# Optimization experiments

Measured on AMD Instinct MI355X. Metric: run time of the kernel, lower is better.

Reference implementation:

```python
import jax, jax.numpy as jnp
import numpy as np

NDIM = (256, 256, 256)
NMIN = (-1.0, -1.0, -1.0)
NMAX = (1.0, 1.0, 1.0)
NDELTA = tuple((NMAX[i] - NMIN[i]) / (NDIM[i] - 1.0) for i in range(3))
MIN_DEG, MAX_DEG = 0, 10
ANNEALED_ALPHA = 1.0
EPS = 1e-12


def compute_grad(grid):
    # central differences on the voxel grid with edge padding -> [N, 3]
    g = grid.reshape(NDIM[0], NDIM[1], NDIM[2])
    p = jnp.pad(g, ((1, 1), (1, 1), (1, 1)), mode='edge')
    dx = (p[2:, 1:-1, 1:-1] - p[:-2, 1:-1, 1:-1]) / (2.0 * NDELTA[0])
    dy = (p[1:-1, 2:, 1:-1] - p[1:-1, :-2, 1:-1]) / (2.0 * NDELTA[1])
    dz = (p[1:-1, 1:-1, 2:] - p[1:-1, 1:-1, :-2]) / (2.0 * NDELTA[2])
    return jnp.stack([dx, dy, dz], axis=-1).reshape(-1, 3)


def trilinear3(data, pts):
    # data: [N, 4] flattened voxel features, pts: [B, 3] -> [B, 4]
    x = (pts[..., 0] - NMIN[0]) / NDELTA[0]
    y = (pts[..., 1] - NMIN[1]) / NDELTA[1]
    z = (pts[..., 2] - NMIN[2]) / NDELTA[2]
    x0f = jnp.floor(x); y0f = jnp.floor(y); z0f = jnp.floor(z)
    xd = (x - x0f)[..., None]
    yd = (y - y0f)[..., None]
    zd = (z - z0f)[..., None]
    x0 = jnp.clip(x0f.astype(jnp.int32), 0, NDIM[0] - 1)
    x1 = jnp.clip(x0f.astype(jnp.int32) + 1, 0, NDIM[0] - 1)
    y0 = jnp.clip(y0f.astype(jnp.int32), 0, NDIM[1] - 1)
    y1 = jnp.clip(y0f.astype(jnp.int32) + 1, 0, NDIM[1] - 1)
    z0 = jnp.clip(z0f.astype(jnp.int32), 0, NDIM[2] - 1)
    z1 = jnp.clip(z0f.astype(jnp.int32) + 1, 0, NDIM[2] - 1)
    sYZ, sZ = NDIM[1] * NDIM[2], NDIM[2]
    gat = lambda i, j, k: data[sYZ * i + sZ * j + k]
    c00 = gat(x0, y0, z0) * (1 - xd) + gat(x1, y0, z0) * xd
    c01 = gat(x0, y0, z1) * (1 - xd) + gat(x1, y0, z1) * xd
    c10 = gat(x0, y1, z0) * (1 - xd) + gat(x1, y1, z0) * xd
    c11 = gat(x0, y1, z1) * (1 - xd) + gat(x1, y1, z1) * xd
    c0 = c00 * (1 - yd) + c10 * yd
    c1 = c01 * (1 - yd) + c11 * yd
    return c0 * (1 - zd) + c1 * zd


def annealed_pos_enc(x, alpha):
    # nerfies-style windowed positional encoding with identity concat
    bands = jnp.arange(MIN_DEG, MAX_DEG, dtype=x.dtype)  # [D]
    scales = 2.0 ** bands
    xb = x[..., None, :] * scales[:, None]               # [..., D, 3]
    four = jnp.sin(jnp.stack([xb, xb + 0.5 * jnp.pi], axis=-2))  # [..., D, 2, 3]
    w = jnp.clip(alpha - bands, 0.0, 1.0)
    w = 0.5 * (1.0 - jnp.cos(jnp.pi * w))                # cosine easing window
    four = four * w[:, None, None]
    four = four.reshape(x.shape[:-1] + (-1,))            # [..., D*6]
    return jnp.concatenate([x, four], axis=-1)           # [..., 3 + D*6]


def mlp(feats, w0, b0, w1, b1, w2, b2, w3, b3, wo, bo):
    # net_depth=4, skip_layer=2 -> concat inputs after layer index 2
    h = jax.nn.relu(feats @ w0 + b0)
    h = jax.nn.relu(h @ w1 + b1)
    h = jax.nn.relu(h @ w2 + b2)
    h = jnp.concatenate([h, feats], axis=-1)
    h = jax.nn.relu(h @ w3 + b3)
    return h @ wo + bo


def safe_l2_norm(v):
    return jnp.sqrt(jnp.sum(v * v, axis=-1, keepdims=True) + EPS)


def setup_inputs() -> dict:
    key = jax.random.key(0)
    ks = jax.random.split(key, 8)
    B = 1048576
    N = NDIM[0] * NDIM[1] * NDIM[2]
    x = jax.random.uniform(ks[0], (B, 3), jnp.float32, -1.0, 1.0)
    grid = jax.random.normal(ks[1], (N, 1), jnp.float32)
    glorot = lambda k, fi, fo: jax.random.normal(k, (fi, fo), jnp.float32) * jnp.sqrt(2.0 / (fi + fo))
    return {
        'x': x, 'grid': grid,
        'w0': glorot(ks[2], 63, 128), 'b0': jnp.zeros((128,), jnp.float32),
        'w1': glorot(ks[3], 128, 128), 'b1': jnp.zeros((128,), jnp.float32),
        'w2': glorot(ks[4], 128, 128), 'b2': jnp.zeros((128,), jnp.float32),
        'w3': glorot(ks[5], 191, 128), 'b3': jnp.zeros((128,), jnp.float32),
        'wo': jax.random.normal(ks[6], (128, 3), jnp.float32) * 1e-5,  # output_init normal(1e-5)
        'bo': jnp.zeros((3,), jnp.float32),
    }


def reference(x, grid, w0, b0, w1, b1, w2, b2, w3, b3, wo, bo):
    data = jnp.concatenate([grid, compute_grad(grid)], axis=-1)  # [N, 4]
    ret = trilinear3(data, x)                                    # [B, 4]
    feats = annealed_pos_enc(x[:, None], ANNEALED_ALPHA * MAX_DEG)  # [B, 1, 63]
    raw = mlp(feats, w0, b0, w1, b1, w2, b2, w3, b3, wo, bo)[:, 0]  # [B, 3]
    # residual + direct output: rotate gradient vector by axis-angle raw
    theta = safe_l2_norm(raw)
    e = raw / theta
    cond = ret[..., 1:]
    a = safe_l2_norm(cond)
    v = cond / a
    rot = a * (jnp.cos(theta) * v + jnp.sin(theta) * jnp.cross(e, v)
               + (1.0 - jnp.cos(theta)) * jnp.sum(e * v, axis=-1, keepdims=True) * e)
    return (ret[..., :1], ret[..., 1:], rot)
```

## Files before the change

### kernel.cpp

```cpp
#include <hip/hip_runtime.h>


typedef __attribute__((ext_vector_type(4))) float f4;
typedef long long llg;
typedef __attribute__((ext_vector_type(2))) long long llg2;

#define MFMA8 __builtin_amdgcn_mfma_f32_16x16x32_fp8_fp8
#define SCHED_FENCE() __builtin_amdgcn_sched_barrier(0)

__device__ __forceinline__ float bf2f(unsigned int u) {
    union { float f; unsigned int i; } v; v.i = u << 16; return v.f;
}
__device__ __forceinline__ unsigned int pkbf(float a, float b) {
    unsigned int r;
    asm("v_cvt_pk_bf16_f32 %0, %1, %2" : "=v"(r) : "v"(a), "v"(b));
    return r;
}
__device__ __forceinline__ float vfract(float a) {
    float d; asm("v_fract_f32 %0, %1" : "=v"(d) : "v"(a)); return d;
}
__device__ __forceinline__ float vsin(float a) {
    float d; asm("v_sin_f32 %0, %1" : "=v"(d) : "v"(a)); return d;
}
__device__ __forceinline__ float gv(const float* __restrict__ g, int i, int j, int k) {
    return g[(i * 256 + j) * 256 + k];
}
__device__ __forceinline__ int featmap(int kp) {
    if (kp < 3) return kp;
    if (kp == 3) return -1;
    const int m = kp - 4, b = m / 6, r = m - 6 * b, d = r >> 1, c = r & 1;
    return 3 + 6 * b + 3 * c + d;
}
__device__ __forceinline__ int hidperm(int k) {
    const int kt = k >> 5, q = (k >> 3) & 3, j = k & 7;
    return 32 * kt + ((j >> 2) << 4) + (q << 2) + (j & 3);
}
__device__ __forceinline__ llg mkllg(unsigned int lo, unsigned int hi) {
    return (llg)(((unsigned long long)lo) | (((unsigned long long)hi) << 32));
}
__device__ __forceinline__ unsigned int pack8(f4 acc) {
    int d = __builtin_amdgcn_cvt_pk_fp8_f32(fmaxf(acc[0], 0.f), fmaxf(acc[1], 0.f), 0, false);
    d     = __builtin_amdgcn_cvt_pk_fp8_f32(fmaxf(acc[2], 0.f), fmaxf(acc[3], 0.f), d, true);
    return (unsigned int)d;
}

#define WS_TOTAL 67584
#define SWZ_BLOCKS 264
#define DG_BLOCKS 8192
#define DG_OFF_SH 131072
#define WS_NEED (262144ull + 16777216ull * 8ull)
#define WO_SCALE 8192.0f
#define WO_INV   (1.0f / 8192.0f)
#define INV2PI 0.15915494309189535f

__global__ __launch_bounds__(256) void prep(
    const float* __restrict__ g,
    const float* __restrict__ w0, const float* __restrict__ w1,
    const float* __restrict__ w2, const float* __restrict__ w3,
    const float* __restrict__ wo,
    unsigned char* __restrict__ ws8, unsigned short* __restrict__ dg,
    int do_dgrid)
{
    const int bid = blockIdx.x;
    if (bid < SWZ_BLOCKS) {
        int idx = bid * 256 + threadIdx.x;
        const float* src; int base, KTP, Kact, Nact, ld;
        if (idx < 8192)       { src = w0; base = 0;     KTP = 1; Kact = 64;  Nact = 128; ld = 128; }
        else if (idx < 24576) { src = w1; base = 8192;  KTP = 2; Kact = 128; Nact = 128; ld = 128; }
        else if (idx < 40960) { src = w2; base = 24576; KTP = 2; Kact = 128; Nact = 128; ld = 128; }
        else if (idx < 65536) { src = w3; base = 40960; KTP = 3; Kact = 192; Nact = 128; ld = 128; }
        else                  { src = wo; base = 65536; KTP = 2; Kact = 128; Nact = 3;   ld = 3;   }
        int local = idx - base;
        int j    = local & 7;
        int half = (local >> 3) & 1;
        int lane = (local >> 4) & 63;
        int c    = local >> 10;
        int ktp  = c % KTP, nt = c / KTP;
        int kt   = ktp * 2 + half;
        int k = kt * 32 + ((lane >> 4) << 3) + j;
        int n = nt * 16 + (lane & 15);
        float v = 0.0f;
        if (k < Kact && n < Nact) {
            int ko;
            if (base == 0) {
                ko = featmap(k);
            } else if (base == 40960) {
                if (k >= 128) {
                    int f = featmap(k - 128);
                    ko = (f < 0) ? -1 : 128 + f;
                } else {
                    ko = hidperm(k);
                }
            } else {
                ko = hidperm(k);
            }
            if (ko >= 0) v = src[ko * ld + n];
            if (base == 65536) v *= WO_SCALE;
        }
        int p = __builtin_amdgcn_cvt_pk_fp8_f32(v, v, 0, false);
        ws8[idx] = (unsigned char)(p & 0xff);
    } else if (do_dgrid) {
        const int t  = (bid - SWZ_BLOCKS) * 256 + threadIdx.x;
        const int k0 = (t & 31) << 3;
        const int j  = (t >> 5) & 255;
        const int i  = t >> 13;
        const float* row = g + (i * 256 + j) * 256;
        const float* rxp = g + (min(i + 1, 255) * 256 + j) * 256;
        const float* rxm = g + (max(i - 1, 0)   * 256 + j) * 256;
        const float* ryp = g + (i * 256 + min(j + 1, 255)) * 256;
        const float* rym = g + (i * 256 + max(j - 1, 0))   * 256;
        float se[8], sxp[8], sxm[8], syp[8], sym[8];
        {
            f4 a = *(const f4*)(row + k0), b = *(const f4*)(row + k0 + 4);
            #pragma unroll
            for (int q = 0; q < 4; ++q) { se[q] = a[q]; se[q + 4] = b[q]; }
            a = *(const f4*)(rxp + k0); b = *(const f4*)(rxp + k0 + 4);
            #pragma unroll
            for (int q = 0; q < 4; ++q) { sxp[q] = a[q]; sxp[q + 4] = b[q]; }
            a = *(const f4*)(rxm + k0); b = *(const f4*)(rxm + k0 + 4);
            #pragma unroll
            for (int q = 0; q < 4; ++q) { sxm[q] = a[q]; sxm[q + 4] = b[q]; }
            a = *(const f4*)(ryp + k0); b = *(const f4*)(ryp + k0 + 4);
            #pragma unroll
            for (int q = 0; q < 4; ++q) { syp[q] = a[q]; syp[q + 4] = b[q]; }
            a = *(const f4*)(rym + k0); b = *(const f4*)(rym + k0 + 4);
            #pragma unroll
            for (int q = 0; q < 4; ++q) { sym[q] = a[q]; sym[q + 4] = b[q]; }
        }
        float zv[10];
        zv[0] = row[max(k0 - 1, 0)];
        #pragma unroll
        for (int q = 0; q < 8; ++q) zv[q + 1] = se[q];
        zv[9] = row[min(k0 + 8, 255)];
        unsigned int o[16];
        #pragma unroll
        for (int q = 0; q < 8; ++q) {
            o[q * 2 + 0] = pkbf(se[q], (sxp[q] - sxm[q]) * 63.75f);
            o[q * 2 + 1] = pkbf((syp[q] - sym[q]) * 63.75f, (zv[q + 2] - zv[q]) * 63.75f);
        }
        unsigned short* dst = dg + (size_t)(((i * 256 + j) * 256 + k0)) * 4;
        #pragma unroll
        for (int q = 0; q < 4; ++q)
            *(uint4*)(dst + q * 8) = *(const uint4*)(&o[q * 4]);
    }
}

#define FSTRIDE_B 88
#define WV_BYTES (32 * FSTRIDE_B)

#define HIDDEN_LAYER(WSL, BIASP, SRCP, DSTP)                                    \
    do {                                                                        \
        _Pragma("unroll")                                                       \
        for (int utp = 0; utp < 4; ++utp) {                                     \
            const int utA = 2 * utp, utB = 2 * utp + 1;                         \
            llg2 wa0 = *(const llg2*)((WSL) + ((utA * 2 + 0) * 64 + lane) * 16);\
            llg2 wa1 = *(const llg2*)((WSL) + ((utA * 2 + 1) * 64 + lane) * 16);\
            llg2 wb0 = *(const llg2*)((WSL) + ((utB * 2 + 0) * 64 + lane) * 16);\
            llg2 wb1 = *(const llg2*)((WSL) + ((utB * 2 + 1) * 64 + lane) * 16);\
            const f4 biasA = *(const f4*)((BIASP) + utA * 16 + quad * 4);       \
            const f4 biasB = *(const f4*)((BIASP) + utB * 16 + quad * 4);       \
            _Pragma("unroll")                                                   \
            for (int pt = 0; pt < 2; ++pt) {                                    \
                f4 a0 = biasA, a1 = biasB;                                      \
                a0 = MFMA8(wa0[0], SRCP[pt][0], a0, 0, 0, 0);                   \
                a0 = MFMA8(wa0[1], SRCP[pt][1], a0, 0, 0, 0);                   \
                a0 = MFMA8(wa1[0], SRCP[pt][2], a0, 0, 0, 0);                   \
                a0 = MFMA8(wa1[1], SRCP[pt][3], a0, 0, 0, 0);                   \
                a1 = MFMA8(wb0[0], SRCP[pt][0], a1, 0, 0, 0);                   \
                a1 = MFMA8(wb0[1], SRCP[pt][1], a1, 0, 0, 0);                   \
                a1 = MFMA8(wb1[0], SRCP[pt][2], a1, 0, 0, 0);                   \
                a1 = MFMA8(wb1[1], SRCP[pt][3], a1, 0, 0, 0);                   \
                DSTP[pt][utp] = mkllg(pack8(a0), pack8(a1));                    \
            }                                                                   \
            SCHED_FENCE();                                                      \
        }                                                                       \
    } while (0)

template<bool FAST>
__global__ __launch_bounds__(256, 5) void voxmlp(
    const float* __restrict__ x, const float* __restrict__ grid,
    const unsigned char* __restrict__ ws8, const unsigned short* __restrict__ dg,
    const float* __restrict__ b0, const float* __restrict__ b1,
    const float* __restrict__ b2, const float* __restrict__ b3,
    const float* __restrict__ bo,
    float* __restrict__ out, int B)
{
    __shared__ unsigned char smem[WV_BYTES * 4];

    const int lane = threadIdx.x & 63;
    const int wave = threadIdx.x >> 6;
    const int quad = lane >> 4;
    const int lm   = lane & 15;
    unsigned char* fbuf = smem + wave * WV_BYTES;

    const int pbase = blockIdx.x * 128 + wave * 32;

    const int p2   = lane & 31;
    const int role = lane >> 5;
    const int pid  = pbase + p2;

    const float px = x[pid * 3 + 0];
    const float py = x[pid * 3 + 1];
    const float pz = x[pid * 3 + 2];

    if (role == 0) {
        const float fx = (px + 1.0f) * 127.5f;
        const float fy = (py + 1.0f) * 127.5f;
        const float fz = (pz + 1.0f) * 127.5f;
        const float fx0 = floorf(fx), fy0 = floorf(fy), fz0 = floorf(fz);
        const float xd = fx - fx0, yd = fy - fy0, zd = fz - fz0;
        const int ix0 = min(max((int)fx0, 0), 255);
        const int iy0 = min(max((int)fy0, 0), 255);
        const int iz0 = min(max((int)fz0, 0), 255);
        const int ix1 = min(ix0 + 1, 255);
        const int iy1 = min(iy0 + 1, 255);
        const int iz1 = min(iz0 + 1, 255);

        float ret0 = 0.f, c1 = 0.f, c2 = 0.f, c3 = 0.f;
        if (FAST) {
            const unsigned char* dgb = (const unsigned char*)dg;
            const unsigned int vbase = (unsigned int)((ix0 * 65536 + iy0 * 256 + iz0) << 3);
            const unsigned int ox = (unsigned int)((ix1 - ix0) << 19);
            const unsigned int oy = (unsigned int)((iy1 - iy0) << 11);
            const unsigned int oz = (unsigned int)((iz1 - iz0) << 3);
            #pragma unroll
            for (int c = 0; c < 8; ++c) {
                const float wgt = ((c & 4) ? xd : 1.0f - xd) *
                                  ((c & 2) ? yd : 1.0f - yd) *
                                  ((c & 1) ? zd : 1.0f - zd);
                const unsigned int off = vbase + ((c & 4) ? ox : 0u)
                                               + ((c & 2) ? oy : 0u)
                                               + ((c & 1) ? oz : 0u);
                const uint2 w = *(const uint2*)(dgb + off);
                ret0 = fmaf(wgt, bf2f(w.x & 0xffffu), ret0);
                c1   = fmaf(wgt, bf2f(w.x >> 16),     c1);
                c2   = fmaf(wgt, bf2f(w.y & 0xffffu), c2);
                c3   = fmaf(wgt, bf2f(w.y >> 16),     c3);
            }
        } else {
            #pragma unroll
            for (int c = 0; c < 8; ++c) {
                const int i = (c & 4) ? ix1 : ix0;
                const int j = (c & 2) ? iy1 : iy0;
                const int k = (c & 1) ? iz1 : iz0;
                const float wgt = ((c & 4) ? xd : 1.0f - xd) *
                                  ((c & 2) ? yd : 1.0f - yd) *
                                  ((c & 1) ? zd : 1.0f - zd);
                const float v  = gv(grid, i, j, k);
                const float gx = (gv(grid, min(i + 1, 255), j, k) - gv(grid, max(i - 1, 0), j, k)) * 63.75f;
                const float gy = (gv(grid, i, min(j + 1, 255), k) - gv(grid, i, max(j - 1, 0), k)) * 63.75f;
                const float gz = (gv(grid, i, j, min(k + 1, 255)) - gv(grid, i, j, max(k - 1, 0))) * 63.75f;
                ret0 = fmaf(wgt, v,  ret0);
                c1   = fmaf(wgt, gx, c1);
                c2   = fmaf(wgt, gy, c2);
                c3   = fmaf(wgt, gz, c3);
            }
        }
        out[pid] = ret0;
        out[B + pid * 3 + 0] = c1;
        out[B + pid * 3 + 1] = c2;
        out[B + pid * 3 + 2] = c3;
        float* cst = (float*)(fbuf + p2 * FSTRIDE_B + 64);
        cst[0] = c1; cst[1] = c2; cst[2] = c3;
    } else {
        const float r0 = px * INV2PI, r1 = py * INV2PI, r2 = pz * INV2PI;
        unsigned char* fb = fbuf + p2 * FSTRIDE_B;
        auto slotv = [&](int n) -> float {
            if (n == 0) return px;
            if (n == 1) return py;
            if (n == 2) return pz;
            if (n == 3) return 0.0f;
            const int m = n - 4, b = m / 6, t = m % 6, ax = t >> 1, ph = t & 1;
            const float rr = (ax == 0) ? r0 : (ax == 1) ? r1 : r2;
            const float arg = rr * (float)(1 << b) + (ph ? 0.25f : 0.0f);
            return vsin(vfract(arg));
        };
        #pragma unroll
        for (int w = 0; w < 8; ++w) {
            int lo = __builtin_amdgcn_cvt_pk_fp8_f32(slotv(8 * w + 0), slotv(8 * w + 1), 0, false);
            lo     = __builtin_amdgcn_cvt_pk_fp8_f32(slotv(8 * w + 2), slotv(8 * w + 3), lo, true);
            int hi = __builtin_amdgcn_cvt_pk_fp8_f32(slotv(8 * w + 4), slotv(8 * w + 5), 0, false);
            hi     = __builtin_amdgcn_cvt_pk_fp8_f32(slotv(8 * w + 6), slotv(8 * w + 7), hi, true);
            uint2 pk; pk.x = (unsigned int)lo; pk.y = (unsigned int)hi;
            *(uint2*)(fb + w * 8) = pk;
        }
    }
    __builtin_amdgcn_s_barrier();

    const int frow0 = lm * FSTRIDE_B + quad * 8;

    llg actA[2][4];
    llg actB[2][4];
    llg ffp[2][2];

    #pragma unroll
    for (int pt = 0; pt < 2; ++pt)
        #pragma unroll
        for (int kt = 0; kt < 2; ++kt)
            ffp[pt][kt] = *(const llg*)(fbuf + pt * 16 * FSTRIDE_B + frow0 + kt * 32);

    #pragma unroll
    for (int utp = 0; utp < 4; ++utp) {
        const int utA = 2 * utp, utB = 2 * utp + 1;
        llg2 wA = *(const llg2*)(ws8 + (utA * 64 + lane) * 16);
        llg2 wB = *(const llg2*)(ws8 + (utB * 64 + lane) * 16);
        const f4 biasA = *(const f4*)(b0 + utA * 16 + quad * 4);
        const f4 biasB = *(const f4*)(b0 + utB * 16 + quad * 4);
        #pragma unroll
        for (int pt = 0; pt < 2; ++pt) {
            f4 a0 = biasA, a1 = biasB;
            a0 = MFMA8(wA[0], ffp[pt][0], a0, 0, 0, 0);
            a0 = MFMA8(wA[1], ffp[pt][1], a0, 0, 0, 0);
            a1 = MFMA8(wB[0], ffp[pt][0], a1, 0, 0, 0);
            a1 = MFMA8(wB[1], ffp[pt][1], a1, 0, 0, 0);
            actA[pt][utp] = mkllg(pack8(a0), pack8(a1));
        }
        SCHED_FENCE();
    }

    HIDDEN_LAYER(ws8 + 8192,  b1, actA, actB);
    HIDDEN_LAYER(ws8 + 24576, b2, actB, actA);

    #pragma unroll
    for (int utp = 0; utp < 4; ++utp) {
        const int utA = 2 * utp, utB = 2 * utp + 1;
        llg2 ha0 = *(const llg2*)(ws8 + 40960 + ((utA * 3 + 0) * 64 + lane) * 16);
        llg2 ha1 = *(const llg2*)(ws8 + 40960 + ((utA * 3 + 1) * 64 + lane) * 16);
        llg2 ha2 = *(const llg2*)(ws8 + 40960 + ((utA * 3 + 2) * 64 + lane) * 16);
        llg2 hb0 = *(const llg2*)(ws8 + 40960 + ((utB * 3 + 0) * 64 + lane) * 16);
        llg2 hb1 = *(const llg2*)(ws8 + 40960 + ((utB * 3 + 1) * 64 + lane) * 16);
        llg2 hb2 = *(const llg2*)(ws8 + 40960 + ((utB * 3 + 2) * 64 + lane) * 16);
        const f4 biasA = *(const f4*)(b3 + utA * 16 + quad * 4);
        const f4 biasB = *(const f4*)(b3 + utB * 16 + quad * 4);
        #pragma unroll
        for (int pt = 0; pt < 2; ++pt) {
            f4 a0 = biasA, a1 = biasB;
            a0 = MFMA8(ha0[0], actA[pt][0], a0, 0, 0, 0);
            a0 = MFMA8(ha0[1], actA[pt][1], a0, 0, 0, 0);
            a0 = MFMA8(ha1[0], actA[pt][2], a0, 0, 0, 0);
            a0 = MFMA8(ha1[1], actA[pt][3], a0, 0, 0, 0);
            a0 = MFMA8(ha2[0], ffp[pt][0],  a0, 0, 0, 0);
            a0 = MFMA8(ha2[1], ffp[pt][1],  a0, 0, 0, 0);
            a1 = MFMA8(hb0[0], actA[pt][0], a1, 0, 0, 0);
            a1 = MFMA8(hb0[1], actA[pt][1], a1, 0, 0, 0);
            a1 = MFMA8(hb1[0], actA[pt][2], a1, 0, 0, 0);
            a1 = MFMA8(hb1[1], actA[pt][3], a1, 0, 0, 0);
            a1 = MFMA8(hb2[0], ffp[pt][0],  a1, 0, 0, 0);
            a1 = MFMA8(hb2[1], ffp[pt][1],  a1, 0, 0, 0);
            actB[pt][utp] = mkllg(pack8(a0), pack8(a1));
        }
        SCHED_FENCE();
    }

    const llg2 o0 = *(const llg2*)(ws8 + 65536 + (lane * 16));
    const llg2 o1 = *(const llg2*)(ws8 + 65536 + ((64 + lane) * 16));

    const float bo0 = bo[0], bo1 = bo[1], bo2 = bo[2];
    #pragma unroll
    for (int pt = 0; pt < 2; ++pt) {
        f4 acc = {0.f, 0.f, 0.f, 0.f};
        acc = MFMA8(o0[0], actB[pt][0], acc, 0, 0, 0);
        acc = MFMA8(o0[1], actB[pt][1], acc, 0, 0, 0);
        acc = MFMA8(o1[0], actB[pt][2], acc, 0, 0, 0);
        acc = MFMA8(o1[1], actB[pt][3], acc, 0, 0, 0);

        const int pp = pt * 16 + lm;
        const float* cst = (const float*)(fbuf + pp * FSTRIDE_B + 64);
        const float g1 = cst[0], g2 = cst[1], g3 = cst[2];
        const float r0 = acc[0] * WO_INV + bo0;
        const float r1 = acc[1] * WO_INV + bo1;
        const float r2 = acc[2] * WO_INV + bo2;
        const float theta = sqrtf(fmaf(r0, r0, fmaf(r1, r1, r2 * r2)) + 1e-12f);
        const float it = __builtin_amdgcn_rcpf(theta);
        const float e0 = r0 * it, e1 = r1 * it, e2 = r2 * it;
        const float a = sqrtf(fmaf(g1, g1, fmaf(g2, g2, g3 * g3)) + 1e-12f);
        const float ia = __builtin_amdgcn_rcpf(a);
        const float v0 = g1 * ia, v1 = g2 * ia, v2 = g3 * ia;
        const float rv = theta * INV2PI;
        const float st = vsin(vfract(rv));
        const float ct = vsin(vfract(rv + 0.25f));
        const float cx = e1 * v2 - e2 * v1;
        const float cy = e2 * v0 - e0 * v2;
        const float cz = e0 * v1 - e1 * v0;
        const float om = (1.0f - ct) * (e0 * v0 + e1 * v1 + e2 * v2);
        if (quad == 0) {
            const int pid2 = pbase + pp;
            out[4 * B + pid2 * 3 + 0] = a * (ct * v0 + st * cx + om * e0);
            out[4 * B + pid2 * 3 + 1] = a * (ct * v1 + st * cy + om * e1);
            out[4 * B + pid2 * 3 + 2] = a * (ct * v2 + st * cz + om * e2);
        }
    }
}

extern "C" void kernel_launch(void* const* d_in, const int* in_sizes, int n_in,
                              void* d_out, int out_size, void* d_ws, size_t ws_size,
                              hipStream_t stream)
{
    const float* x    = (const float*)d_in[0];
    const float* grid = (const float*)d_in[1];
    const float* w0   = (const float*)d_in[2];
    const float* b0   = (const float*)d_in[3];
    const float* w1   = (const float*)d_in[4];
    const float* b1   = (const float*)d_in[5];
    const float* w2   = (const float*)d_in[6];
    const float* b2   = (const float*)d_in[7];
    const float* w3   = (const float*)d_in[8];
    const float* b3   = (const float*)d_in[9];
    const float* wo   = (const float*)d_in[10];
    const float* bo   = (const float*)d_in[11];
    float* out = (float*)d_out;
    unsigned char* ws8 = (unsigned char*)d_ws;
    unsigned short* dg = (unsigned short*)d_ws + DG_OFF_SH;

    const int B = in_sizes[0] / 3;
    const int fast = (ws_size >= WS_NEED) ? 1 : 0;
    const int nprep = fast ? (SWZ_BLOCKS + DG_BLOCKS) : SWZ_BLOCKS;
    prep<<<nprep, 256, 0, stream>>>(grid, w0, w1, w2, w3, wo, ws8, dg, fast);
    if (fast)
        voxmlp<true><<<B / 128, 256, 0, stream>>>(x, grid, ws8, dg, b0, b1, b2, b3, bo, out, B);
    else
        voxmlp<false><<<B / 128, 256, 0, stream>>>(x, grid, ws8, dg, b0, b1, b2, b3, bo, out, B);
}
```

Measured before the change: 322.1 us.

## Switch MLP matmuls to 16x16x128 scaled FP8 MFMA with new weight layout

Replaces the 16x16x32 FP8 MFMA chains with the gfx950 16x16x128 f8f6f4 scaled MFMA, so each output tile needs one instruction per 128-wide K block instead of four chained ones. The prep kernel re-swizzles the weights into 32-byte-per-lane fragments with a new hidden-unit permutation. The feature row is widened and zero-padded to 128 bytes, with a new ordering for the positional-encoding features. This cuts MFMA issue count and accumulator dependency chains. In exchange, layer 0 and the feature half of layer 3 now multiply zero padding from 64 up to 128, and the feature buffer takes more LDS.

```diff
diff --git a/kernel.cpp b/kernel.cpp
--- a/kernel.cpp
+++ b/kernel.cpp
@@ -4,8 +4,10 @@
 typedef __attribute__((ext_vector_type(4))) float f4;
 typedef long long llg;
 typedef __attribute__((ext_vector_type(2))) long long llg2;
-
-#define MFMA8 __builtin_amdgcn_mfma_f32_16x16x32_fp8_fp8
+typedef __attribute__((ext_vector_type(8))) int v8i;
+
+#define MFMASC(A,B,C) \
+    __builtin_amdgcn_mfma_scale_f32_16x16x128_f8f6f4((A),(B),(C),0,0,0,0x7f,0,0x7f)
 #define SCHED_FENCE() __builtin_amdgcn_sched_barrier(0)
 
 __device__ __forceinline__ float bf2f(unsigned int u) {
@@ -25,27 +27,29 @@
 __device__ __forceinline__ float gv(const float* __restrict__ g, int i, int j, int k) {
     return g[(i * 256 + j) * 256 + k];
 }
-__device__ __forceinline__ int featmap(int kp) {
-    if (kp < 3) return kp;
-    if (kp == 3) return -1;
-    const int m = kp - 4, b = m / 6, r = m - 6 * b, d = r >> 1, c = r & 1;
-    return 3 + 6 * b + 3 * c + d;
-}
-__device__ __forceinline__ int hidperm(int k) {
-    const int kt = k >> 5, q = (k >> 3) & 3, j = k & 7;
-    return 32 * kt + ((j >> 2) << 4) + (q << 2) + (j & 3);
-}
-__device__ __forceinline__ llg mkllg(unsigned int lo, unsigned int hi) {
-    return (llg)(((unsigned long long)lo) | (((unsigned long long)hi) << 32));
+__device__ __forceinline__ int hidperm2(int k) {
+    const int q = k >> 5, m = k & 31, t = m >> 2, j = m & 3;
+    return 16 * t + 4 * q + j;
 }
 __device__ __forceinline__ unsigned int pack8(f4 acc) {
     int d = __builtin_amdgcn_cvt_pk_fp8_f32(fmaxf(acc[0], 0.f), fmaxf(acc[1], 0.f), 0, false);
     d     = __builtin_amdgcn_cvt_pk_fp8_f32(fmaxf(acc[2], 0.f), fmaxf(acc[3], 0.f), d, true);
     return (unsigned int)d;
 }
-
-#define WS_TOTAL 67584
-#define SWZ_BLOCKS 264
+__device__ __forceinline__ v8i ldv8(const unsigned char* p) {
+    union { v8i v; llg2 h[2]; } u;
+    u.h[0] = *(const llg2*)(p);
+    u.h[1] = *(const llg2*)(p + 16);
+    return u.v;
+}
+
+#define L0OFF 0
+#define L1OFF 16384
+#define L2OFF 32768
+#define L3OFF 49152
+#define OUTOFF 81920
+#define WS_TOTAL 83968
+#define SWZ_BLOCKS 328
 #define DG_BLOCKS 8192
 #define DG_OFF_SH 131072
 #define WS_NEED (262144ull + 16777216ull * 8ull)
@@ -64,38 +68,30 @@
     const int bid = blockIdx.x;
     if (bid < SWZ_BLOCKS) {
         int idx = bid * 256 + threadIdx.x;
-        const float* src; int base, KTP, Kact, Nact, ld;
-        if (idx < 8192)       { src = w0; base = 0;     KTP = 1; Kact = 64;  Nact = 128; ld = 128; }
-        else if (idx < 24576) { src = w1; base = 8192;  KTP = 2; Kact = 128; Nact = 128; ld = 128; }
-        else if (idx < 40960) { src = w2; base = 24576; KTP = 2; Kact = 128; Nact = 128; ld = 128; }
-        else if (idx < 65536) { src = w3; base = 40960; KTP = 3; Kact = 192; Nact = 128; ld = 128; }
-        else                  { src = wo; base = 65536; KTP = 2; Kact = 128; Nact = 3;   ld = 3;   }
+        const float* src; int base, KT;
+        if (idx < 16384)      { src = w0; base = L0OFF;  KT = 1; }
+        else if (idx < 32768) { src = w1; base = L1OFF;  KT = 1; }
+        else if (idx < 49152) { src = w2; base = L2OFF;  KT = 1; }
+        else if (idx < 81920) { src = w3; base = L3OFF;  KT = 2; }
+        else                  { src = wo; base = OUTOFF; KT = 1; }
         int local = idx - base;
-        int j    = local & 7;
-        int half = (local >> 3) & 1;
-        int lane = (local >> 4) & 63;
-        int c    = local >> 10;
-        int ktp  = c % KTP, nt = c / KTP;
-        int kt   = ktp * 2 + half;
-        int k = kt * 32 + ((lane >> 4) << 3) + j;
+        int m    = local & 31;
+        int lane = (local >> 5) & 63;
+        int tile = local >> 11;
+        int kb   = (KT == 2) ? (tile & 1) : 0;
+        int nt   = (KT == 2) ? (tile >> 1) : tile;
+        int k = kb * 128 + ((lane >> 4) << 5) + m;
         int n = nt * 16 + (lane & 15);
         float v = 0.0f;
-        if (k < Kact && n < Nact) {
-            int ko;
-            if (base == 0) {
-                ko = featmap(k);
-            } else if (base == 40960) {
-                if (k >= 128) {
-                    int f = featmap(k - 128);
-                    ko = (f < 0) ? -1 : 128 + f;
-                } else {
-                    ko = hidperm(k);
-                }
-            } else {
-                ko = hidperm(k);
-            }
-            if (ko >= 0) v = src[ko * ld + n];
-            if (base == 65536) v *= WO_SCALE;
+        if (base == L0OFF) {
+            if (k < 63) v = src[k * 128 + n];
+        } else if (base == L3OFF) {
+            if (kb == 0) v = src[hidperm2(k) * 128 + n];
+            else { int f = k - 128; if (f < 63) v = src[(128 + f) * 128 + n]; }
+        } else if (base == OUTOFF) {
+            if (n < 3) v = src[hidperm2(k) * 3 + n] * WO_SCALE;
+        } else {
+            v = src[hidperm2(k) * 128 + n];
         }
         int p = __builtin_amdgcn_cvt_pk_fp8_f32(v, v, 0, false);
         ws8[idx] = (unsigned char)(p & 0xff);
@@ -145,36 +141,8 @@
     }
 }
 
-#define FSTRIDE_B 88
+#define FSTRIDE_B 144
 #define WV_BYTES (32 * FSTRIDE_B)
-
-#define HIDDEN_LAYER(WSL, BIASP, SRCP, DSTP)                                    \
-    do {                                                                        \
-        _Pragma("unroll")                                                       \
-        for (int utp = 0; utp < 4; ++utp) {                                     \
-            const int utA = 2 * utp, utB = 2 * utp + 1;                         \
-            llg2 wa0 = *(const llg2*)((WSL) + ((utA * 2 + 0) * 64 + lane) * 16);\
-            llg2 wa1 = *(const llg2*)((WSL) + ((utA * 2 + 1) * 64 + lane) * 16);\
-            llg2 wb0 = *(const llg2*)((WSL) + ((utB * 2 + 0) * 64 + lane) * 16);\
-            llg2 wb1 = *(const llg2*)((WSL) + ((utB * 2 + 1) * 64 + lane) * 16);\
-            const f4 biasA = *(const f4*)((BIASP) + utA * 16 + quad * 4);       \
-            const f4 biasB = *(const f4*)((BIASP) + utB * 16 + quad * 4);       \
-            _Pragma("unroll")                                                   \
-            for (int pt = 0; pt < 2; ++pt) {                                    \
-                f4 a0 = biasA, a1 = biasB;                                      \
-                a0 = MFMA8(wa0[0], SRCP[pt][0], a0, 0, 0, 0);                   \
-                a0 = MFMA8(wa0[1], SRCP[pt][1], a0, 0, 0, 0);                   \
-                a0 = MFMA8(wa1[0], SRCP[pt][2], a0, 0, 0, 0);                   \
-                a0 = MFMA8(wa1[1], SRCP[pt][3], a0, 0, 0, 0);                   \
-                a1 = MFMA8(wb0[0], SRCP[pt][0], a1, 0, 0, 0);                   \
-                a1 = MFMA8(wb0[1], SRCP[pt][1], a1, 0, 0, 0);                   \
-                a1 = MFMA8(wb1[0], SRCP[pt][2], a1, 0, 0, 0);                   \
-                a1 = MFMA8(wb1[1], SRCP[pt][3], a1, 0, 0, 0);                   \
-                DSTP[pt][utp] = mkllg(pack8(a0), pack8(a1));                    \
-            }                                                                   \
-            SCHED_FENCE();                                                      \
-        }                                                                       \
-    } while (0)
 
 template<bool FAST>
 __global__ __launch_bounds__(256, 5) void voxmlp(
@@ -260,7 +228,7 @@
         out[B + pid * 3 + 0] = c1;
         out[B + pid * 3 + 1] = c2;
         out[B + pid * 3 + 2] = c3;
-        float* cst = (float*)(fbuf + p2 * FSTRIDE_B + 64);
+        float* cst = (float*)(fbuf + p2 * FSTRIDE_B + 128);
         cst[0] = c1; cst[1] = c2; cst[2] = c3;
     } else {
         const float r0 = px * INV2PI, r1 = py * INV2PI, r2 = pz * INV2PI;
@@ -269,11 +237,10 @@
             if (n == 0) return px;
             if (n == 1) return py;
             if (n == 2) return pz;
-            if (n == 3) return 0.0f;
-            const int m = n - 4, b = m / 6, t = m % 6, ax = t >> 1, ph = t & 1;
-            const float rr = (ax == 0) ? r0 : (ax == 1) ? r1 : r2;
-            const float arg = rr * (float)(1 << b) + (ph ? 0.25f : 0.0f);
-            return vsin(vfract(arg));
+            if (n >= 63) return 0.0f;
+            const int m = n - 3, b = m / 6, rem = m % 6, s = rem / 3, d = rem % 3;
+            const float rr = (d == 0) ? r0 : (d == 1) ? r1 : r2;
+            return vsin(vfract(rr * (float)(1 << b) + (s ? 0.25f : 0.0f)));
         };
         #pragma unroll
         for (int w = 0; w < 8; ++w) {
@@ -284,88 +251,79 @@
             uint2 pk; pk.x = (unsigned int)lo; pk.y = (unsigned int)hi;
             *(uint2*)(fb + w * 8) = pk;
         }
+        const uint4 z = {0u, 0u, 0u, 0u};
+        #pragma unroll
+        for (int w = 0; w < 4; ++w) *(uint4*)(fb + 64 + w * 16) = z;
     }
     __builtin_amdgcn_s_barrier();
 
-    const int frow0 = lm * FSTRIDE_B + quad * 8;
-
-    llg actA[2][4];
-    llg actB[2][4];
-    llg ffp[2][2];
+    const int frow = lm * FSTRIDE_B + quad * 32;
+
+    v8i actA, actAq;
+    v8i actB, actBq;
+
+    {
+        const v8i f0 = ldv8(fbuf + frow);
+        const v8i f1 = ldv8(fbuf + 16 * FSTRIDE_B + frow);
+        #pragma unroll
+        for (int ut = 0; ut < 8; ++ut) {
+            const v8i w = ldv8(ws8 + L0OFF + (ut * 64 + lane) * 32);
+            const f4 bias = *(const f4*)(b0 + ut * 16 + quad * 4);
+            f4 a0 = MFMASC(w, f0, bias);
+            f4 a1 = MFMASC(w, f1, bias);
+            actA[ut]  = (int)pack8(a0);
+            actAq[ut] = (int)pack8(a1);
+            SCHED_FENCE();
+        }
+    }
 
     #pragma unroll
-    for (int pt = 0; pt < 2; ++pt)
-        #pragma unroll
-        for (int kt = 0; kt < 2; ++kt)
-            ffp[pt][kt] = *(const llg*)(fbuf + pt * 16 * FSTRIDE_B + frow0 + kt * 32);
+    for (int ut = 0; ut < 8; ++ut) {
+        const v8i w = ldv8(ws8 + L1OFF + (ut * 64 + lane) * 32);
+        const f4 bias = *(const f4*)(b1 + ut * 16 + quad * 4);
+        f4 a0 = MFMASC(w, actA,  bias);
+        f4 a1 = MFMASC(w, actAq, bias);
+        actB[ut]  = (int)pack8(a0);
+        actBq[ut] = (int)pack8(a1);
+        SCHED_FENCE();
+    }
 
     #pragma unroll
-    for (int utp = 0; utp < 4; ++utp) {
-        const int utA = 2 * utp, utB = 2 * utp + 1;
-        llg2 wA = *(const llg2*)(ws8 + (utA * 64 + lane) * 16);
-        llg2 wB = *(const llg2*)(ws8 + (utB * 64 + lane) * 16);
-        const f4 biasA = *(const f4*)(b0 + utA * 16 + quad * 4);
-        const f4 biasB = *(const f4*)(b0 + utB * 16 + quad * 4);
-        #pragma unroll
-        for (int pt = 0; pt < 2; ++pt) {
-            f4 a0 = biasA, a1 = biasB;
-            a0 = MFMA8(wA[0], ffp[pt][0], a0, 0, 0, 0);
-            a0 = MFMA8(wA[1], ffp[pt][1], a0, 0, 0, 0);
-            a1 = MFMA8(wB[0], ffp[pt][0], a1, 0, 0, 0);
-            a1 = MFMA8(wB[1], ffp[pt][1], a1, 0, 0, 0);
-            actA[pt][utp] = mkllg(pack8(a0), pack8(a1));
-        }
+    for (int ut = 0; ut < 8; ++ut) {
+        const v8i w = ldv8(ws8 + L2OFF + (ut * 64 + lane) * 32);
+        const f4 bias = *(const f4*)(b2 + ut * 16 + quad * 4);
+        f4 a0 = MFMASC(w, actB,  bias);
+        f4 a1 = MFMASC(w, actBq, bias);
+        actA[ut]  = (int)pack8(a0);
+        actAq[ut] = (int)pack8(a1);
         SCHED_FENCE();
     }
 
-    HIDDEN_LAYER(ws8 + 8192,  b1, actA, actB);
-    HIDDEN_LAYER(ws8 + 24576, b2, actB, actA);
-
-    #pragma unroll
-    for (int utp = 0; utp < 4; ++utp) {
-        const int utA = 2 * utp, utB = 2 * utp + 1;
-        llg2 ha0 = *(const llg2*)(ws8 + 40960 + ((utA * 3 + 0) * 64 + lane) * 16);
-        llg2 ha1 = *(const llg2*)(ws8 + 40960 + ((utA * 3 + 1) * 64 + lane) * 16);
-        llg2 ha2 = *(const llg2*)(ws8 + 40960 + ((utA * 3 + 2) * 64 + lane) * 16);
-        llg2 hb0 = *(const llg2*)(ws8 + 40960 + ((utB * 3 + 0) * 64 + lane) * 16);
-        llg2 hb1 = *(const llg2*)(ws8 + 40960 + ((utB * 3 + 1) * 64 + lane) * 16);
-        llg2 hb2 = *(const llg2*)(ws8 + 40960 + ((utB * 3 + 2) * 64 + lane) * 16);
-        const f4 biasA = *(const f4*)(b3 + utA * 16 + quad * 4);
-        const f4 biasB = *(const f4*)(b3 + utB * 16 + quad * 4);
-        #pragma unroll
-        for (int pt = 0; pt < 2; ++pt) {
-            f4 a0 = biasA, a1 = biasB;
-            a0 = MFMA8(ha0[0], actA[pt][0], a0, 0, 0, 0);
-            a0 = MFMA8(ha0[1], actA[pt][1], a0, 0, 0, 0);
-            a0 = MFMA8(ha1[0], actA[pt][2], a0, 0, 0, 0);
-            a0 = MFMA8(ha1[1], actA[pt][3], a0, 0, 0, 0);
-            a0 = MFMA8(ha2[0], ffp[pt][0],  a0, 0, 0, 0);
-            a0 = MFMA8(ha2[1], ffp[pt][1],  a0, 0, 0, 0);
-            a1 = MFMA8(hb0[0], actA[pt][0], a1, 0, 0, 0);
-            a1 = MFMA8(hb0[1], actA[pt][1], a1, 0, 0, 0);
-            a1 = MFMA8(hb1[0], actA[pt][2], a1, 0, 0, 0);
-            a1 = MFMA8(hb1[1], actA[pt][3], a1, 0, 0, 0);
-            a1 = MFMA8(hb2[0], ffp[pt][0],  a1, 0, 0, 0);
-            a1 = MFMA8(hb2[1], ffp[pt][1],  a1, 0, 0, 0);
-            actB[pt][utp] = mkllg(pack8(a0), pack8(a1));
-        }
-        SCHED_FENCE();
-    }
-
-    const llg2 o0 = *(const llg2*)(ws8 + 65536 + (lane * 16));
-    const llg2 o1 = *(const llg2*)(ws8 + 65536 + ((64 + lane) * 16));
-
+    {
+        const v8i f0 = ldv8(fbuf + frow);
+        const v8i f1 = ldv8(fbuf + 16 * FSTRIDE_B + frow);
+        #pragma unroll
+        for (int ut = 0; ut < 8; ++ut) {
+            const v8i wh = ldv8(ws8 + L3OFF + ((ut * 2 + 0) * 64 + lane) * 32);
+            const v8i wt = ldv8(ws8 + L3OFF + ((ut * 2 + 1) * 64 + lane) * 32);
+            const f4 bias = *(const f4*)(b3 + ut * 16 + quad * 4);
+            f4 a0 = MFMASC(wh, actA,  bias); a0 = MFMASC(wt, f0, a0);
+            f4 a1 = MFMASC(wh, actAq, bias); a1 = MFMASC(wt, f1, a1);
+            actB[ut]  = (int)pack8(a0);
+            actBq[ut] = (int)pack8(a1);
+            SCHED_FENCE();
+        }
+    }
+
+    const v8i wout = ldv8(ws8 + OUTOFF + lane * 32);
     const float bo0 = bo[0], bo1 = bo[1], bo2 = bo[2];
     #pragma unroll
     for (int pt = 0; pt < 2; ++pt) {
         f4 acc = {0.f, 0.f, 0.f, 0.f};
-        acc = MFMA8(o0[0], actB[pt][0], acc, 0, 0, 0);
-        acc = MFMA8(o0[1], actB[pt][1], acc, 0, 0, 0);
-        acc = MFMA8(o1[0], actB[pt][2], acc, 0, 0, 0);
-        acc = MFMA8(o1[1], actB[pt][3], acc, 0, 0, 0);
+        acc = MFMASC(wout, pt ? actBq : actB, acc);
 
         const int pp = pt * 16 + lm;
-        const float* cst = (const float*)(fbuf + pp * FSTRIDE_B + 64);
+        const float* cst = (const float*)(fbuf + pp * FSTRIDE_B + 128);
         const float g1 = cst[0], g2 = cst[1], g3 = cst[2];
         const float r0 = acc[0] * WO_INV + bo0;
         const float r1 = acc[1] * WO_INV + bo1;
```

Result: slower. 349.0 us (+8.3%).

## Balance gather and encoding work across wave halves; halve dgrid prep blocks

Applied to the files above, without the earlier changes.

Before, half of each wave did the 8-corner trilinear gather while the other half computed the sinusoidal feature encoding, so the two halves ran divergent paths. Now both halves do the gather, each taking four corners (one x-slab), and combine partial sums with a cross-lane xor shuffle; then both halves compute half of the encoding slots. The intent is to remove divergence and balance latency between the two lane groups. Separately, the derived-grid prep now runs half as many blocks, each thread processing two voxel rows, which cuts launch and scheduling overhead but lowers parallelism in that phase.

```diff
diff --git a/kernel.cpp b/kernel.cpp
--- a/kernel.cpp
+++ b/kernel.cpp
@@ -46,12 +46,58 @@
 
 #define WS_TOTAL 67584
 #define SWZ_BLOCKS 264
-#define DG_BLOCKS 8192
+#define DG_BLOCKS 4096
 #define DG_OFF_SH 131072
 #define WS_NEED (262144ull + 16777216ull * 8ull)
 #define WO_SCALE 8192.0f
 #define WO_INV   (1.0f / 8192.0f)
 #define INV2PI 0.15915494309189535f
+
+__device__ __forceinline__ void dg_one(const float* __restrict__ g,
+                                       unsigned short* __restrict__ dg, int t)
+{
+    const int k0 = (t & 31) << 3;
+    const int j  = (t >> 5) & 255;
+    const int i  = t >> 13;
+    const float* row = g + (i * 256 + j) * 256;
+    const float* rxp = g + (min(i + 1, 255) * 256 + j) * 256;
+    const float* rxm = g + (max(i - 1, 0)   * 256 + j) * 256;
+    const float* ryp = g + (i * 256 + min(j + 1, 255)) * 256;
+    const float* rym = g + (i * 256 + max(j - 1, 0))   * 256;
+    float se[8], sxp[8], sxm[8], syp[8], sym[8];
+    {
+        f4 a = *(const f4*)(row + k0), b = *(const f4*)(row + k0 + 4);
+        #pragma unroll
+        for (int q = 0; q < 4; ++q) { se[q] = a[q]; se[q + 4] = b[q]; }
+        a = *(const f4*)(rxp + k0); b = *(const f4*)(rxp + k0 + 4);
+        #pragma unroll
+        for (int q = 0; q < 4; ++q) { sxp[q] = a[q]; sxp[q + 4] = b[q]; }
+        a = *(const f4*)(rxm + k0); b = *(const f4*)(rxm + k0 + 4);
+        #pragma unroll
+        for (int q = 0; q < 4; ++q) { sxm[q] = a[q]; sxm[q + 4] = b[q]; }
+        a = *(const f4*)(ryp + k0); b = *(const f4*)(ryp + k0 + 4);
+        #pragma unroll
+        for (int q = 0; q < 4; ++q) { syp[q] = a[q]; syp[q + 4] = b[q]; }
+        a = *(const f4*)(rym + k0); b = *(const f4*)(rym + k0 + 4);
+        #pragma unroll
+        for (int q = 0; q < 4; ++q) { sym[q] = a[q]; sym[q + 4] = b[q]; }
+    }
+    float zv[10];
+    zv[0] = row[max(k0 - 1, 0)];
+    #pragma unroll
+    for (int q = 0; q < 8; ++q) zv[q + 1] = se[q];
+    zv[9] = row[min(k0 + 8, 255)];
+    unsigned int o[16];
+    #pragma unroll
+    for (int q = 0; q < 8; ++q) {
+        o[q * 2 + 0] = pkbf(se[q], (sxp[q] - sxm[q]) * 63.75f);
+        o[q * 2 + 1] = pkbf((syp[q] - sym[q]) * 63.75f, (zv[q + 2] - zv[q]) * 63.75f);
+    }
+    unsigned short* dst = dg + (size_t)(((i * 256 + j) * 256 + k0)) * 4;
+    #pragma unroll
+    for (int q = 0; q < 4; ++q)
+        *(uint4*)(dst + q * 8) = *(const uint4*)(&o[q * 4]);
+}
 
 __global__ __launch_bounds__(256) void prep(
     const float* __restrict__ g,
@@ -100,48 +146,9 @@
         int p = __builtin_amdgcn_cvt_pk_fp8_f32(v, v, 0, false);
         ws8[idx] = (unsigned char)(p & 0xff);
     } else if (do_dgrid) {
-        const int t  = (bid - SWZ_BLOCKS) * 256 + threadIdx.x;
-        const int k0 = (t & 31) << 3;
-        const int j  = (t >> 5) & 255;
-        const int i  = t >> 13;
-        const float* row = g + (i * 256 + j) * 256;
-        const float* rxp = g + (min(i + 1, 255) * 256 + j) * 256;
-        const float* rxm = g + (max(i - 1, 0)   * 256 + j) * 256;
-        const float* ryp = g + (i * 256 + min(j + 1, 255)) * 256;
-        const float* rym = g + (i * 256 + max(j - 1, 0))   * 256;
-        float se[8], sxp[8], sxm[8], syp[8], sym[8];
-        {
-            f4 a = *(const f4*)(row + k0), b = *(const f4*)(row + k0 + 4);
-            #pragma unroll
-            for (int q = 0; q < 4; ++q) { se[q] = a[q]; se[q + 4] = b[q]; }
-            a = *(const f4*)(rxp + k0); b = *(const f4*)(rxp + k0 + 4);
-            #pragma unroll
-            for (int q = 0; q < 4; ++q) { sxp[q] = a[q]; sxp[q + 4] = b[q]; }
-            a = *(const f4*)(rxm + k0); b = *(const f4*)(rxm + k0 + 4);
-            #pragma unroll
-            for (int q = 0; q < 4; ++q) { sxm[q] = a[q]; sxm[q + 4] = b[q]; }
-            a = *(const f4*)(ryp + k0); b = *(const f4*)(ryp + k0 + 4);
-            #pragma unroll
-            for (int q = 0; q < 4; ++q) { syp[q] = a[q]; syp[q + 4] = b[q]; }
-            a = *(const f4*)(rym + k0); b = *(const f4*)(rym + k0 + 4);
-            #pragma unroll
-            for (int q = 0; q < 4; ++q) { sym[q] = a[q]; sym[q + 4] = b[q]; }
-        }
-        float zv[10];
-        zv[0] = row[max(k0 - 1, 0)];
-        #pragma unroll
-        for (int q = 0; q < 8; ++q) zv[q + 1] = se[q];
-        zv[9] = row[min(k0 + 8, 255)];
-        unsigned int o[16];
-        #pragma unroll
-        for (int q = 0; q < 8; ++q) {
-            o[q * 2 + 0] = pkbf(se[q], (sxp[q] - sxm[q]) * 63.75f);
-            o[q * 2 + 1] = pkbf((syp[q] - sym[q]) * 63.75f, (zv[q + 2] - zv[q]) * 63.75f);
-        }
-        unsigned short* dst = dg + (size_t)(((i * 256 + j) * 256 + k0)) * 4;
-        #pragma unroll
-        for (int q = 0; q < 4; ++q)
-            *(uint4*)(dst + q * 8) = *(const uint4*)(&o[q * 4]);
+        const int t0 = (bid - SWZ_BLOCKS) * 256 + threadIdx.x;
+        dg_one(g, dg, t0);
+        dg_one(g, dg, t0 + DG_BLOCKS * 256);
     }
 }
 
@@ -196,14 +203,14 @@
     const int pbase = blockIdx.x * 128 + wave * 32;
 
     const int p2   = lane & 31;
-    const int role = lane >> 5;
+    const int half = lane >> 5;
     const int pid  = pbase + p2;
 
     const float px = x[pid * 3 + 0];
     const float py = x[pid * 3 + 1];
     const float pz = x[pid * 3 + 2];
 
-    if (role == 0) {
+    {
         const float fx = (px + 1.0f) * 127.5f;
         const float fy = (py + 1.0f) * 127.5f;
         const float fz = (pz + 1.0f) * 127.5f;
@@ -215,22 +222,21 @@
         const int ix1 = min(ix0 + 1, 255);
         const int iy1 = min(iy0 + 1, 255);
         const int iz1 = min(iz0 + 1, 255);
+        const float wx = half ? xd : 1.0f - xd;
 
         float ret0 = 0.f, c1 = 0.f, c2 = 0.f, c3 = 0.f;
         if (FAST) {
             const unsigned char* dgb = (const unsigned char*)dg;
-            const unsigned int vbase = (unsigned int)((ix0 * 65536 + iy0 * 256 + iz0) << 3);
-            const unsigned int ox = (unsigned int)((ix1 - ix0) << 19);
+            const unsigned int vb = (unsigned int)((ix0 * 65536 + iy0 * 256 + iz0) << 3)
+                                  + (half ? (unsigned int)((ix1 - ix0) << 19) : 0u);
             const unsigned int oy = (unsigned int)((iy1 - iy0) << 11);
             const unsigned int oz = (unsigned int)((iz1 - iz0) << 3);
             #pragma unroll
-            for (int c = 0; c < 8; ++c) {
-                const float wgt = ((c & 4) ? xd : 1.0f - xd) *
-                                  ((c & 2) ? yd : 1.0f - yd) *
-                                  ((c & 1) ? zd : 1.0f - zd);
-                const unsigned int off = vbase + ((c & 4) ? ox : 0u)
-                                               + ((c & 2) ? oy : 0u)
-                                               + ((c & 1) ? oz : 0u);
+            for (int c = 0; c < 4; ++c) {
+                const float wgt = wx * ((c & 2) ? yd : 1.0f - yd) *
+                                       ((c & 1) ? zd : 1.0f - zd);
+                const unsigned int off = vb + ((c & 2) ? oy : 0u)
+                                            + ((c & 1) ? oz : 0u);
                 const uint2 w = *(const uint2*)(dgb + off);
                 ret0 = fmaf(wgt, bf2f(w.x & 0xffffu), ret0);
                 c1   = fmaf(wgt, bf2f(w.x >> 16),     c1);
@@ -238,14 +244,13 @@
                 c3   = fmaf(wgt, bf2f(w.y >> 16),     c3);
             }
         } else {
+            const int i = half ? ix1 : ix0;
             #pragma unroll
-            for (int c = 0; c < 8; ++c) {
-                const int i = (c & 4) ? ix1 : ix0;
+            for (int c = 0; c < 4; ++c) {
                 const int j = (c & 2) ? iy1 : iy0;
                 const int k = (c & 1) ? iz1 : iz0;
-                const float wgt = ((c & 4) ? xd : 1.0f - xd) *
-                                  ((c & 2) ? yd : 1.0f - yd) *
-                                  ((c & 1) ? zd : 1.0f - zd);
+                const float wgt = wx * ((c & 2) ? yd : 1.0f - yd) *
+                                       ((c & 1) ? zd : 1.0f - zd);
                 const float v  = gv(grid, i, j, k);
                 const float gx = (gv(grid, min(i + 1, 255), j, k) - gv(grid, max(i - 1, 0), j, k)) * 63.75f;
                 const float gy = (gv(grid, i, min(j + 1, 255), k) - gv(grid, i, max(j - 1, 0), k)) * 63.75f;
@@ -256,13 +261,21 @@
                 c3   = fmaf(wgt, gz, c3);
             }
         }
-        out[pid] = ret0;
-        out[B + pid * 3 + 0] = c1;
-        out[B + pid * 3 + 1] = c2;
-        out[B + pid * 3 + 2] = c3;
-        float* cst = (float*)(fbuf + p2 * FSTRIDE_B + 64);
-        cst[0] = c1; cst[1] = c2; cst[2] = c3;
-    } else {
+        ret0 += __shfl_xor(ret0, 32);
+        c1   += __shfl_xor(c1, 32);
+        c2   += __shfl_xor(c2, 32);
+        c3   += __shfl_xor(c3, 32);
+        if (half == 0) {
+            out[pid] = ret0;
+            out[B + pid * 3 + 0] = c1;
+            out[B + pid * 3 + 1] = c2;
+            out[B + pid * 3 + 2] = c3;
+            float* cst = (float*)(fbuf + p2 * FSTRIDE_B + 64);
+            cst[0] = c1; cst[1] = c2; cst[2] = c3;
+        }
+    }
+
+    {
         const float r0 = px * INV2PI, r1 = py * INV2PI, r2 = pz * INV2PI;
         unsigned char* fb = fbuf + p2 * FSTRIDE_B;
         auto slotv = [&](int n) -> float {
@@ -276,13 +289,14 @@
             return vsin(vfract(arg));
         };
         #pragma unroll
-        for (int w = 0; w < 8; ++w) {
-            int lo = __builtin_amdgcn_cvt_pk_fp8_f32(slotv(8 * w + 0), slotv(8 * w + 1), 0, false);
-            lo     = __builtin_amdgcn_cvt_pk_fp8_f32(slotv(8 * w + 2), slotv(8 * w + 3), lo, true);
-            int hi = __builtin_amdgcn_cvt_pk_fp8_f32(slotv(8 * w + 4), slotv(8 * w + 5), 0, false);
-            hi     = __builtin_amdgcn_cvt_pk_fp8_f32(slotv(8 * w + 6), slotv(8 * w + 7), hi, true);
+        for (int w = 0; w < 4; ++w) {
+            const int s0 = half * 32 + w * 8;
+            int lo = __builtin_amdgcn_cvt_pk_fp8_f32(slotv(s0 + 0), slotv(s0 + 1), 0, false);
+            lo     = __builtin_amdgcn_cvt_pk_fp8_f32(slotv(s0 + 2), slotv(s0 + 3), lo, true);
+            int hi = __builtin_amdgcn_cvt_pk_fp8_f32(slotv(s0 + 4), slotv(s0 + 5), 0, false);
+            hi     = __builtin_amdgcn_cvt_pk_fp8_f32(slotv(s0 + 6), slotv(s0 + 7), hi, true);
             uint2 pk; pk.x = (unsigned int)lo; pk.y = (unsigned int)hi;
-            *(uint2*)(fb + w * 8) = pk;
+            *(uint2*)(fb + (half * 4 + w) * 8) = pk;
         }
     }
     __builtin_amdgcn_s_barrier();
```

After: 390.2 us. +21.1%, slower.

## Stage grid rows in LDS to reuse y-neighbors in gradient prep

Applied to the files above, without the earlier changes.

Restructures the gradient-grid prep so each block handles a 32-wide k-slab across all 256 j rows of one i plane. Each thread stages its center row in shared memory, and the y-neighbor values are read from LDS instead of being fetched again from global memory. This cuts the redundant global loads of y+1/y-1 rows. It adds a __syncthreads, a 36 KB LDS allocation to the whole prep kernel (including the weight-swizzle blocks), and fewer, larger blocks.

```diff
diff --git a/kernel.cpp b/kernel.cpp
--- a/kernel.cpp
+++ b/kernel.cpp
@@ -46,12 +46,13 @@
 
 #define WS_TOTAL 67584
 #define SWZ_BLOCKS 264
-#define DG_BLOCKS 8192
+#define DG_BLOCKS 2048
 #define DG_OFF_SH 131072
 #define WS_NEED (262144ull + 16777216ull * 8ull)
 #define WO_SCALE 8192.0f
 #define WO_INV   (1.0f / 8192.0f)
 #define INV2PI 0.15915494309189535f
+#define LROW 36
 
 __global__ __launch_bounds__(256) void prep(
     const float* __restrict__ g,
@@ -61,6 +62,7 @@
     unsigned char* __restrict__ ws8, unsigned short* __restrict__ dg,
     int do_dgrid)
 {
+    __shared__ float lds[256 * LROW];
     const int bid = blockIdx.x;
     if (bid < SWZ_BLOCKS) {
         int idx = bid * 256 + threadIdx.x;
@@ -100,48 +102,66 @@
         int p = __builtin_amdgcn_cvt_pk_fp8_f32(v, v, 0, false);
         ws8[idx] = (unsigned char)(p & 0xff);
     } else if (do_dgrid) {
-        const int t  = (bid - SWZ_BLOCKS) * 256 + threadIdx.x;
-        const int k0 = (t & 31) << 3;
-        const int j  = (t >> 5) & 255;
-        const int i  = t >> 13;
-        const float* row = g + (i * 256 + j) * 256;
-        const float* rxp = g + (min(i + 1, 255) * 256 + j) * 256;
-        const float* rxm = g + (max(i - 1, 0)   * 256 + j) * 256;
-        const float* ryp = g + (i * 256 + min(j + 1, 255)) * 256;
-        const float* rym = g + (i * 256 + max(j - 1, 0))   * 256;
-        float se[8], sxp[8], sxm[8], syp[8], sym[8];
-        {
-            f4 a = *(const f4*)(row + k0), b = *(const f4*)(row + k0 + 4);
-            #pragma unroll
-            for (int q = 0; q < 4; ++q) { se[q] = a[q]; se[q + 4] = b[q]; }
-            a = *(const f4*)(rxp + k0); b = *(const f4*)(rxp + k0 + 4);
-            #pragma unroll
-            for (int q = 0; q < 4; ++q) { sxp[q] = a[q]; sxp[q + 4] = b[q]; }
-            a = *(const f4*)(rxm + k0); b = *(const f4*)(rxm + k0 + 4);
-            #pragma unroll
-            for (int q = 0; q < 4; ++q) { sxm[q] = a[q]; sxm[q + 4] = b[q]; }
-            a = *(const f4*)(ryp + k0); b = *(const f4*)(ryp + k0 + 4);
-            #pragma unroll
-            for (int q = 0; q < 4; ++q) { syp[q] = a[q]; syp[q + 4] = b[q]; }
-            a = *(const f4*)(rym + k0); b = *(const f4*)(rym + k0 + 4);
-            #pragma unroll
-            for (int q = 0; q < 4; ++q) { sym[q] = a[q]; sym[q + 4] = b[q]; }
-        }
-        float zv[10];
-        zv[0] = row[max(k0 - 1, 0)];
-        #pragma unroll
-        for (int q = 0; q < 8; ++q) zv[q + 1] = se[q];
-        zv[9] = row[min(k0 + 8, 255)];
-        unsigned int o[16];
-        #pragma unroll
-        for (int q = 0; q < 8; ++q) {
-            o[q * 2 + 0] = pkbf(se[q], (sxp[q] - sxm[q]) * 63.75f);
-            o[q * 2 + 1] = pkbf((syp[q] - sym[q]) * 63.75f, (zv[q + 2] - zv[q]) * 63.75f);
-        }
-        unsigned short* dst = dg + (size_t)(((i * 256 + j) * 256 + k0)) * 4;
-        #pragma unroll
-        for (int q = 0; q < 4; ++q)
-            *(uint4*)(dst + q * 8) = *(const uint4*)(&o[q * 4]);
+        const int rb = bid - SWZ_BLOCKS;
+        const int i  = rb >> 3;
+        const int k0 = (rb & 7) << 5;
+        const int j  = threadIdx.x;
+        const float* row = g + (i * 256 + j) * 256 + k0;
+        const float* rxp = g + (min(i + 1, 255) * 256 + j) * 256 + k0;
+        const float* rxm = g + (max(i - 1, 0)   * 256 + j) * 256 + k0;
+        float* myrow = lds + j * LROW;
+
+        #pragma unroll
+        for (int s = 0; s < 8; ++s)
+            *(f4*)(myrow + s * 4) = *(const f4*)(row + s * 4);
+        const float zlo = (k0 == 0)   ? row[0]  : row[-1];
+        const float zhi = (k0 == 224) ? row[31] : row[32];
+        __syncthreads();
+
+        const float* ypr = lds + min(j + 1, 255) * LROW;
+        const float* ymr = lds + max(j - 1, 0)   * LROW;
+        unsigned short* dst = dg + (size_t)((i * 256 + j) * 256 + k0) * 4;
+
+        #pragma unroll
+        for (int s = 0; s < 4; ++s) {
+            const f4 xp0 = *(const f4*)(rxp + s * 8);
+            const f4 xp1 = *(const f4*)(rxp + s * 8 + 4);
+            const f4 xm0 = *(const f4*)(rxm + s * 8);
+            const f4 xm1 = *(const f4*)(rxm + s * 8 + 4);
+            const f4 yp0 = *(const f4*)(ypr + s * 8);
+            const f4 yp1 = *(const f4*)(ypr + s * 8 + 4);
+            const f4 ym0 = *(const f4*)(ymr + s * 8);
+            const f4 ym1 = *(const f4*)(ymr + s * 8 + 4);
+            const f4 c0  = *(const f4*)(myrow + s * 8);
+            const f4 c1  = *(const f4*)(myrow + s * 8 + 4);
+            const float zm = (s == 0) ? zlo : myrow[s * 8 - 1];
+            const float zp = (s == 3) ? zhi : myrow[s * 8 + 8];
+
+            float cen[8], xpv[8], xmv[8], ypv[8], ymv[8];
+            #pragma unroll
+            for (int q = 0; q < 4; ++q) {
+                cen[q] = c0[q];  cen[q + 4] = c1[q];
+                xpv[q] = xp0[q]; xpv[q + 4] = xp1[q];
+                xmv[q] = xm0[q]; xmv[q + 4] = xm1[q];
+                ypv[q] = yp0[q]; ypv[q + 4] = yp1[q];
+                ymv[q] = ym0[q]; ymv[q + 4] = ym1[q];
+            }
+            float z[10];
+            z[0] = zm;
+            #pragma unroll
+            for (int q = 0; q < 8; ++q) z[q + 1] = cen[q];
+            z[9] = zp;
+
+            unsigned int o[16];
+            #pragma unroll
+            for (int q = 0; q < 8; ++q) {
+                o[q * 2 + 0] = pkbf(cen[q], (xpv[q] - xmv[q]) * 63.75f);
+                o[q * 2 + 1] = pkbf((ypv[q] - ymv[q]) * 63.75f, (z[q + 2] - z[q]) * 63.75f);
+            }
+            #pragma unroll
+            for (int q = 0; q < 4; ++q)
+                *(uint4*)(dst + s * 32 + q * 8) = *(const uint4*)(&o[q * 4]);
+        }
     }
 }
 
```

After: 337.9 us. 4.9% more time.
